# Kernel tuning notes

Hardware: AMD Instinct MI355X
Metric: run time of the kernel (lower is better)

The kernel has to match this reference:

```python
import jax, jax.numpy as jnp
import numpy as np

B, C, H, W, K = 32, 256, 32, 32, 1024
BETA = 0.25

def setup_inputs() -> dict:
    key = jax.random.key(0)
    k1, k2 = jax.random.split(key)
    z = jax.random.normal(k1, (B, C, H, W), dtype=jnp.float32)
    # torch init: uniform(-1/K, 1/K)
    embedding = jax.random.uniform(k2, (K, C), dtype=jnp.float32,
                                   minval=-1.0 / K, maxval=1.0 / K)
    return {"z": z, "embedding": embedding}

def reference(z, embedding):
    b, c, h, w = z.shape
    k = embedding.shape[0]
    # permute to [b,h,w,c] (contiguous)
    z_p = jnp.transpose(z, (0, 2, 3, 1))
    # Faithful to the torch code: the [b,h,w,c] contiguous buffer is .view()'d
    # as [b,1,c,h,w]; numpy/jnp reshape of the transposed array matches that.
    zz = z_p.reshape(b, c, h * w)                     # [b,c,hw] (reinterpreted)
    e = jax.lax.stop_gradient(embedding)              # torch uses .data here
    # ||e - z||^2 via dot-product trick, avoids [b,k,c,h,w] intermediate
    dist = (jnp.sum(e * e, axis=1)[None, :, None]
            + jnp.sum(zz * zz, axis=1)[:, None, :]
            - 2.0 * jnp.einsum('kc,bcn->bkn', e, zz))  # [b,k,hw]
    idx = jnp.argmin(dist, axis=1).reshape(b, h, w)    # [b,h,w]
    z_q = embedding[idx]                               # [b,h,w,c]
    loss = (jnp.mean((jax.lax.stop_gradient(z_q) - z_p) ** 2)
            + BETA * jnp.mean((z_q - jax.lax.stop_gradient(z_p)) ** 2))
    # straight-through estimator
    z_q_st = z_p + jax.lax.stop_gradient(z_q - z_p)
    return jnp.transpose(z_q_st, (0, 3, 1, 2)), idx, loss
```

## Files before the change

### kernel.cpp

```cpp
#include <hip/hip_runtime.h>
#include <stdint.h>

#define ZSIZE   8388608
#define NPIX    32768
#define IDX_OFF ZSIZE
#define LOSS_OFF (ZSIZE + NPIX)
#define ET_OFF  1024
#define E1_OFF  263168
#define ZT_OFF  394240
#define CAP     24
#define WWIN    6.0e-3f

using v8s = __attribute__((ext_vector_type(8))) short;
using v4f = __attribute__((ext_vector_type(4))) float;

__device__ __forceinline__ unsigned short bf16rne(float f) {
  unsigned u = __float_as_uint(f);
  return (unsigned short)((u + 0x7FFFu + ((u >> 16) & 1u)) >> 16);
}

__global__ __launch_bounds__(256) void ktr(const float* __restrict__ E,
                                           float* __restrict__ out) {
  __shared__ float tile[64][65];
  const int k0 = blockIdx.x * 64;
  const int c0 = blockIdx.y * 64;
  const int t = threadIdx.x;
  #pragma unroll
  for (int i = 0; i < 4; i++) {
    int f = t + 256 * i;
    int r = f >> 4, q = f & 15;
    float4 e = *(const float4*)(E + (k0 + r) * 256 + c0 + 4 * q);
    tile[r][4 * q + 0] = e.x; tile[r][4 * q + 1] = e.y;
    tile[r][4 * q + 2] = e.z; tile[r][4 * q + 3] = e.w;
  }
  __syncthreads();
  #pragma unroll
  for (int i = 0; i < 4; i++) {
    int f = t + 256 * i;
    int cr = f >> 4, kq = f & 15;
    float4 o;
    o.x = tile[4 * kq + 0][cr];
    o.y = tile[4 * kq + 1][cr];
    o.z = tile[4 * kq + 2][cr];
    o.w = tile[4 * kq + 3][cr];
    *(float4*)(out + ET_OFF + (c0 + cr) * 1024 + k0 + 4 * kq) = o;
  }
}

__global__ __launch_bounds__(256) void kse(float* __restrict__ out) {
  const int k = blockIdx.x * 256 + threadIdx.x;
  const float* Et = out + ET_OFF;
  float acc = 0.0f;
  #pragma unroll 8
  for (int c = 0; c < 256; c++) {
    float v = Et[c * 1024 + k];
    acc = __fadd_rn(acc, __fmul_rn(v, v));
  }
  out[k] = acc;
}

__global__ __launch_bounds__(256) void kes(const float* __restrict__ E,
                                           float* __restrict__ out) {
  unsigned short* e1s = (unsigned short*)(out + E1_OFF);
  const int tile = blockIdx.x;
  const int t = threadIdx.x;
  #pragma unroll
  for (int i = 0; i < 2; i++) {
    int chunk = t + 256 * i;
    int s = chunk >> 6, lane = chunk & 63;
    int r = lane & 15, h = (lane >> 4) & 3;
    const float* src = E + (16 * tile + r) * 256 + 8 * h + 32 * s;
    unsigned short o[8];
    #pragma unroll
    for (int j = 0; j < 8; j++) o[j] = bf16rne(src[j]);
    *(uint4*)(e1s + (size_t)tile * 4096 + (size_t)chunk * 8) = *(const uint4*)o;
  }
}

__global__ __launch_bounds__(256) void kzt(const float* __restrict__ z,
                                           float* __restrict__ out) {
  __shared__ float tile[16][1028];
  unsigned short* zt = (unsigned short*)(out + ZT_OFF);
  const int mg = blockIdx.x;
  const int b  = blockIdx.y;
  const int t = threadIdx.x;
  #pragma unroll
  for (int i = 0; i < 16; i++) {
    float4 v = *(const float4*)(z + (size_t)b * 262144 + (size_t)(mg * 16 + i) * 1024 + 4 * t);
    *(float4*)&tile[i][4 * t] = v;
  }
  __syncthreads();
  const int m = t & 15, w0 = (t >> 4) & 3;
  const int n = w0 * 256 + mg * 16 + m;
  #pragma unroll
  for (int i = 0; i < 8; i++) {
    int g = 4 * i + (t >> 6);
    int c0 = 8 * g;
    unsigned short o[8];
    #pragma unroll
    for (int j = 0; j < 8; j++)
      o[j] = bf16rne(tile[m][4 * (c0 + j) + w0]);
    *(uint4*)(zt + ((size_t)(b * 1024 + n)) * 256 + c0) = *(const uint4*)o;
  }
}

__global__ __launch_bounds__(256, 2) void kmain(const float* __restrict__ z,
                                                const float* __restrict__ E,
                                                float* __restrict__ out) {
  __shared__ __attribute__((aligned(16))) float szs[64];
  __shared__ __attribute__((aligned(16))) float dmins[64];
  __shared__ int   candK[64 * CAP];
  __shared__ float candD[64 * CAP];
  __shared__ int   cnt[64];

  const int t = threadIdx.x;
  const int ccg = blockIdx.x, b = blockIdx.y;
  const int cc0 = ccg * 16;
  const int lane = t & 63, w = t >> 6;
  const int r = t & 15, h = (t >> 4) & 3;
  const int w16r = w * 16 + r;
  const float* zb = z + (size_t)b * 262144;
  const float* se_g = out;
  const unsigned short* e1s = (const unsigned short*)(out + E1_OFF);
  const unsigned short* zt = (const unsigned short*)(out + ZT_OFF);

  if (t < 64) { cnt[t] = 0; dmins[t] = 3.4e38f; }

  if (lane < 16) {
    const int p = w * 16 + lane;
    const float* zp = zb + (cc0 + (p >> 2)) * 1024 + (p & 3);
    float a = 0.0f;
    #pragma unroll 8
    for (int c = 0; c < 256; c++) {
      float v = zp[4 * c];
      a = __fadd_rn(a, __fmul_rn(v, v));
    }
    szs[p] = a;
  }
  __syncthreads();

  float se16r[16];
  #pragma unroll
  for (int ti = 0; ti < 16; ti++) se16r[ti] = se_g[ti * 64 + w16r];

  #pragma unroll 1
  for (int Tp = 0; Tp < 2; Tp++) {
    const int T0 = 2 * Tp, T1 = T0 + 1;
    v8s A0[8], A1[8];
    {
      const unsigned short* a0p =
          zt + ((size_t)(b * 1024 + T0 * 256 + cc0 + r)) * 256 + 8 * h;
      const unsigned short* a1p = a0p + 256 * 256;
      #pragma unroll
      for (int s = 0; s < 8; s++) {
        A0[s] = *(const v8s*)(a0p + 32 * s);
        A1[s] = *(const v8s*)(a1p + 32 * s);
      }
    }
    float sz0[4], sz1[4], b0[4], b1[4];
    #pragma unroll
    for (int reg = 0; reg < 4; reg++) {
      sz0[reg] = szs[16 * h + 4 * reg + T0];
      sz1[reg] = szs[16 * h + 4 * reg + T1];
      b0[reg] = 3.4e38f; b1[reg] = 3.4e38f;
    }

    #pragma unroll 4
    for (int ti = 0; ti < 16; ti++) {
      const unsigned short* bb = e1s + (size_t)(4 * ti + w) * 4096 + (size_t)lane * 8;
      v4f acc0 = (v4f){0.f, 0.f, 0.f, 0.f};
      v4f acc1 = (v4f){0.f, 0.f, 0.f, 0.f};
      #pragma unroll
      for (int s = 0; s < 8; s++) {
        v8s B_ = *(const v8s*)(bb + 512 * s);
        acc0 = __builtin_amdgcn_mfma_f32_16x16x32_bf16(A0[s], B_, acc0, 0, 0, 0);
        acc1 = __builtin_amdgcn_mfma_f32_16x16x32_bf16(A1[s], B_, acc1, 0, 0, 0);
      }
      float se_l = se16r[ti];
      #pragma unroll
      for (int reg = 0; reg < 4; reg++) {
        b0[reg] = fminf(b0[reg], (se_l + sz0[reg]) - 2.0f * acc0[reg]);
        b1[reg] = fminf(b1[reg], (se_l + sz1[reg]) - 2.0f * acc1[reg]);
      }
    }
    #pragma unroll
    for (int reg = 0; reg < 4; reg++) {
      atomicMin((int*)&dmins[16 * h + 4 * reg + T0], __float_as_int(b0[reg]));
      atomicMin((int*)&dmins[16 * h + 4 * reg + T1], __float_as_int(b1[reg]));
    }
  }
  __syncthreads();

  #pragma unroll 1
  for (int Tp = 0; Tp < 2; Tp++) {
    const int T0 = 2 * Tp, T1 = T0 + 1;
    v8s A0[8], A1[8];
    {
      const unsigned short* a0p =
          zt + ((size_t)(b * 1024 + T0 * 256 + cc0 + r)) * 256 + 8 * h;
      const unsigned short* a1p = a0p + 256 * 256;
      #pragma unroll
      for (int s = 0; s < 8; s++) {
        A0[s] = *(const v8s*)(a0p + 32 * s);
        A1[s] = *(const v8s*)(a1p + 32 * s);
      }
    }
    float sz0[4], sz1[4], th0[4], th1[4];
    #pragma unroll
    for (int reg = 0; reg < 4; reg++) {
      sz0[reg] = szs[16 * h + 4 * reg + T0];
      sz1[reg] = szs[16 * h + 4 * reg + T1];
      th0[reg] = dmins[16 * h + 4 * reg + T0] + WWIN;
      th1[reg] = dmins[16 * h + 4 * reg + T1] + WWIN;
    }

    #pragma unroll 4
    for (int ti = 0; ti < 16; ti++) {
      const unsigned short* bb = e1s + (size_t)(4 * ti + w) * 4096 + (size_t)lane * 8;
      v4f acc0 = (v4f){0.f, 0.f, 0.f, 0.f};
      v4f acc1 = (v4f){0.f, 0.f, 0.f, 0.f};
      #pragma unroll
      for (int s = 0; s < 8; s++) {
        v8s B_ = *(const v8s*)(bb + 512 * s);
        acc0 = __builtin_amdgcn_mfma_f32_16x16x32_bf16(A0[s], B_, acc0, 0, 0, 0);
        acc1 = __builtin_amdgcn_mfma_f32_16x16x32_bf16(A1[s], B_, acc1, 0, 0, 0);
      }
      float se_l = se16r[ti];
      const int kl = ti * 64 + w16r;
      #pragma unroll
      for (int reg = 0; reg < 4; reg++) {
        float dd0 = (se_l + sz0[reg]) - 2.0f * acc0[reg];
        if (dd0 <= th0[reg]) {
          int p = 16 * h + 4 * reg + T0;
          int o = atomicAdd(&cnt[p], 1);
          if (o < CAP) { candK[p * CAP + o] = kl; candD[p * CAP + o] = dd0; }
        }
        float dd1 = (se_l + sz1[reg]) - 2.0f * acc1[reg];
        if (dd1 <= th1[reg]) {
          int p = 16 * h + 4 * reg + T1;
          int o = atomicAdd(&cnt[p], 1);
          if (o < CAP) { candK[p * CAP + o] = kl; candD[p * CAP + o] = dd1; }
        }
      }
    }
  }
  __syncthreads();

  for (int i = t; i < 64 * CAP; i += 256) {
    int p = i / CAP, slot = i - p * CAP;
    int cn = cnt[p];
    if (cn > CAP || slot >= cn) continue;
    int k = candK[i];
    const float* er = E + (size_t)k * 256;
    const float* zp = zb + (cc0 + (p >> 2)) * 1024 + (p & 3);
    float dot = 0.0f;
    #pragma unroll 8
    for (int c = 0; c < 256; c++)
      dot = __fmaf_rn(zp[4 * c], er[c], dot);
    candD[i] = __fsub_rn(__fadd_rn(se_g[k], szs[p]), __fmul_rn(2.0f, dot));
  }
  __syncthreads();

  if (t < 64) {
    int p = t, cn = cnt[p];
    if (cn <= CAP) {
      float bd = 3.4e38f; int bi = 0x7FFFFFFF;
      for (int s2 = 0; s2 < cn; s2++) {
        float d2 = candD[p * CAP + s2]; int k2 = candK[p * CAP + s2];
        if (d2 < bd || (d2 == bd && k2 < bi)) { bd = d2; bi = k2; }
      }
      int rr = p >> 2, w0 = p & 3;
      out[IDX_OFF + b * 1024 + (w0 * 256 + cc0 + rr)] = (float)bi;
    }
  }

  for (int p = 0; p < 64; p++) {
    if (cnt[p] > CAP && (p & 3) == w) {
      const float* zp = zb + (cc0 + (p >> 2)) * 1024 + (p & 3);
      float bd = 3.4e38f; int bi = 0x7FFFFFFF;
      for (int k = lane; k < 1024; k += 64) {
        const float* er = E + (size_t)k * 256;
        float dot = 0.0f;
        #pragma unroll 8
        for (int c = 0; c < 256; c++)
          dot = __fmaf_rn(zp[4 * c], er[c], dot);
        float d2 = __fsub_rn(__fadd_rn(se_g[k], szs[p]), __fmul_rn(2.0f, dot));
        if (d2 < bd || (d2 == bd && k < bi)) { bd = d2; bi = k; }
      }
      #pragma unroll
      for (int mm = 32; mm >= 1; mm >>= 1) {
        float d2 = __shfl_xor(bd, mm, 64);
        int i2 = __shfl_xor(bi, mm, 64);
        if (d2 < bd || (d2 == bd && i2 < bi)) { bd = d2; bi = i2; }
      }
      if (lane == 0) {
        int rr = p >> 2, w0 = p & 3;
        out[IDX_OFF + b * 1024 + (w0 * 256 + cc0 + rr)] = (float)bi;
      }
    }
  }
}

__global__ __launch_bounds__(256) void kout(const float* __restrict__ z,
                                            const float* __restrict__ E,
                                            float* __restrict__ out,
                                            float* __restrict__ ws) {
  __shared__ float red[4];
  const int t = threadIdx.x;
  const size_t g4 = (size_t)blockIdx.x * 256 + t;
  const size_t g = g4 * 4;
  const int b = (int)(g >> 18);
  const int c = (int)((g >> 10) & 255);
  const int n = (int)(g & 1023);

  float4 zp = *(const float4*)(z + g);
  float4 idxf = *(const float4*)(out + IDX_OFF + b * 1024 + n);
  int i0 = (int)idxf.x, i1 = (int)idxf.y, i2 = (int)idxf.z, i3 = (int)idxf.w;
  float q0 = E[i0 * 256 + c];
  float q1 = E[i1 * 256 + c];
  float q2 = E[i2 * 256 + c];
  float q3 = E[i3 * 256 + c];
  float d0 = __fsub_rn(q0, zp.x);
  float d1 = __fsub_rn(q1, zp.y);
  float d2 = __fsub_rn(q2, zp.z);
  float d3 = __fsub_rn(q3, zp.w);
  float4 o;
  o.x = __fadd_rn(zp.x, d0);
  o.y = __fadd_rn(zp.y, d1);
  o.z = __fadd_rn(zp.z, d2);
  o.w = __fadd_rn(zp.w, d3);
  *(float4*)(out + g) = o;

  float s = d0 * d0 + d1 * d1 + d2 * d2 + d3 * d3;
  #pragma unroll
  for (int off = 32; off > 0; off >>= 1) s += __shfl_down(s, off);
  if ((t & 63) == 0) red[t >> 6] = s;
  __syncthreads();
  if (t == 0) ws[blockIdx.x] = red[0] + red[1] + red[2] + red[3];
}

__global__ __launch_bounds__(256) void kfin(const float* __restrict__ ws,
                                            float* __restrict__ out) {
  __shared__ float red[4];
  const int t = threadIdx.x;
  float s = 0.0f;
  #pragma unroll
  for (int i = 0; i < 32; i++) s += ws[t + 256 * i];
  #pragma unroll
  for (int off = 32; off > 0; off >>= 1) s += __shfl_down(s, off);
  if ((t & 63) == 0) red[t >> 6] = s;
  __syncthreads();
  if (t == 0) {
    float S = red[0] + red[1] + red[2] + red[3];
    float m = S / 8388608.0f;
    out[LOSS_OFF] = __fadd_rn(m, __fmul_rn(0.25f, m));
  }
}

extern "C" void kernel_launch(void* const* d_in, const int* in_sizes, int n_in,
                              void* d_out, int out_size, void* d_ws, size_t ws_size,
                              hipStream_t stream) {
  const float* z = (const float*)d_in[0];
  const float* E = (const float*)d_in[1];
  float* out = (float*)d_out;
  float* ws = (float*)d_ws;

  ktr<<<dim3(16, 4), 256, 0, stream>>>(E, out);
  kse<<<dim3(4), 256, 0, stream>>>(out);
  kes<<<dim3(64), 256, 0, stream>>>(E, out);
  kzt<<<dim3(16, 32), 256, 0, stream>>>(z, out);
  kmain<<<dim3(16, 32), 256, 0, stream>>>(z, E, out);
  kout<<<dim3(8192), 256, 0, stream>>>(z, E, out, ws);
  kfin<<<dim3(1), 256, 0, stream>>>(ws, out);
}
```

Baseline: 304.4 us.

## Double kmain block to 512 threads and precompute pixel norms in kzt

```diff
diff --git a/kernel.cpp b/kernel.cpp
--- a/kernel.cpp
+++ b/kernel.cpp
@@ -8,6 +8,7 @@
 #define ET_OFF  1024
 #define E1_OFF  263168
 #define ZT_OFF  394240
+#define SZ_OFF  4588544
 #define CAP     24
 #define WWIN    6.0e-3f
 
@@ -81,6 +82,7 @@
                                            float* __restrict__ out) {
   __shared__ float tile[16][1028];
   unsigned short* zt = (unsigned short*)(out + ZT_OFF);
+  float* szg = out + SZ_OFF;
   const int mg = blockIdx.x;
   const int b  = blockIdx.y;
   const int t = threadIdx.x;
@@ -102,9 +104,19 @@
       o[j] = bf16rne(tile[m][4 * (c0 + j) + w0]);
     *(uint4*)(zt + ((size_t)(b * 1024 + n)) * 256 + c0) = *(const uint4*)o;
   }
-}
-
-__global__ __launch_bounds__(256, 2) void kmain(const float* __restrict__ z,
+  if (t < 64) {
+    const int ms = t >> 2, ws = t & 3;
+    float a = 0.0f;
+    #pragma unroll 8
+    for (int c = 0; c < 256; c++) {
+      float v = tile[ms][4 * c + ws];
+      a = __fadd_rn(a, __fmul_rn(v, v));
+    }
+    szg[b * 1024 + ws * 256 + mg * 16 + ms] = a;
+  }
+}
+
+__global__ __launch_bounds__(512, 2) void kmain(const float* __restrict__ z,
                                                 const float* __restrict__ E,
                                                 float* __restrict__ out) {
   __shared__ __attribute__((aligned(16))) float szs[64];
@@ -116,26 +128,20 @@
   const int t = threadIdx.x;
   const int ccg = blockIdx.x, b = blockIdx.y;
   const int cc0 = ccg * 16;
-  const int lane = t & 63, w = t >> 6;
+  const int lane = t & 63;
+  const int w = (t >> 6) & 3;
+  const int Tp = t >> 8;
   const int r = t & 15, h = (t >> 4) & 3;
   const int w16r = w * 16 + r;
   const float* zb = z + (size_t)b * 262144;
   const float* se_g = out;
   const unsigned short* e1s = (const unsigned short*)(out + E1_OFF);
   const unsigned short* zt = (const unsigned short*)(out + ZT_OFF);
-
-  if (t < 64) { cnt[t] = 0; dmins[t] = 3.4e38f; }
-
-  if (lane < 16) {
-    const int p = w * 16 + lane;
-    const float* zp = zb + (cc0 + (p >> 2)) * 1024 + (p & 3);
-    float a = 0.0f;
-    #pragma unroll 8
-    for (int c = 0; c < 256; c++) {
-      float v = zp[4 * c];
-      a = __fadd_rn(a, __fmul_rn(v, v));
-    }
-    szs[p] = a;
+  const float* szg = out + SZ_OFF;
+
+  if (t < 64) {
+    cnt[t] = 0; dmins[t] = 3.4e38f;
+    szs[t] = szg[b * 1024 + (t & 3) * 256 + cc0 + (t >> 2)];
   }
   __syncthreads();
 
@@ -143,27 +149,30 @@
   #pragma unroll
   for (int ti = 0; ti < 16; ti++) se16r[ti] = se_g[ti * 64 + w16r];
 
-  #pragma unroll 1
-  for (int Tp = 0; Tp < 2; Tp++) {
-    const int T0 = 2 * Tp, T1 = T0 + 1;
-    v8s A0[8], A1[8];
-    {
-      const unsigned short* a0p =
-          zt + ((size_t)(b * 1024 + T0 * 256 + cc0 + r)) * 256 + 8 * h;
-      const unsigned short* a1p = a0p + 256 * 256;
-      #pragma unroll
-      for (int s = 0; s < 8; s++) {
-        A0[s] = *(const v8s*)(a0p + 32 * s);
-        A1[s] = *(const v8s*)(a1p + 32 * s);
-      }
-    }
-    float sz0[4], sz1[4], b0[4], b1[4];
-    #pragma unroll
-    for (int reg = 0; reg < 4; reg++) {
-      sz0[reg] = szs[16 * h + 4 * reg + T0];
-      sz1[reg] = szs[16 * h + 4 * reg + T1];
-      b0[reg] = 3.4e38f; b1[reg] = 3.4e38f;
-    }
+  const int T0 = 2 * Tp, T1 = T0 + 1;
+
+  v8s A0[8], A1[8];
+  {
+    const unsigned short* a0p =
+        zt + ((size_t)(b * 1024 + T0 * 256 + cc0 + r)) * 256 + 8 * h;
+    const unsigned short* a1p = a0p + 256 * 256;
+    #pragma unroll
+    for (int s = 0; s < 8; s++) {
+      A0[s] = *(const v8s*)(a0p + 32 * s);
+      A1[s] = *(const v8s*)(a1p + 32 * s);
+    }
+  }
+  float sz0[4], sz1[4];
+  #pragma unroll
+  for (int reg = 0; reg < 4; reg++) {
+    sz0[reg] = szs[16 * h + 4 * reg + T0];
+    sz1[reg] = szs[16 * h + 4 * reg + T1];
+  }
+
+  {
+    float b0[4], b1[4];
+    #pragma unroll
+    for (int reg = 0; reg < 4; reg++) { b0[reg] = 3.4e38f; b1[reg] = 3.4e38f; }
 
     #pragma unroll 4
     for (int ti = 0; ti < 16; ti++) {
@@ -191,25 +200,10 @@
   }
   __syncthreads();
 
-  #pragma unroll 1
-  for (int Tp = 0; Tp < 2; Tp++) {
-    const int T0 = 2 * Tp, T1 = T0 + 1;
-    v8s A0[8], A1[8];
-    {
-      const unsigned short* a0p =
-          zt + ((size_t)(b * 1024 + T0 * 256 + cc0 + r)) * 256 + 8 * h;
-      const unsigned short* a1p = a0p + 256 * 256;
-      #pragma unroll
-      for (int s = 0; s < 8; s++) {
-        A0[s] = *(const v8s*)(a0p + 32 * s);
-        A1[s] = *(const v8s*)(a1p + 32 * s);
-      }
-    }
-    float sz0[4], sz1[4], th0[4], th1[4];
+  {
+    float th0[4], th1[4];
     #pragma unroll
     for (int reg = 0; reg < 4; reg++) {
-      sz0[reg] = szs[16 * h + 4 * reg + T0];
-      sz1[reg] = szs[16 * h + 4 * reg + T1];
       th0[reg] = dmins[16 * h + 4 * reg + T0] + WWIN;
       th1[reg] = dmins[16 * h + 4 * reg + T1] + WWIN;
     }
@@ -246,7 +240,7 @@
   }
   __syncthreads();
 
-  for (int i = t; i < 64 * CAP; i += 256) {
+  for (int i = t; i < 64 * CAP; i += 512) {
     int p = i / CAP, slot = i - p * CAP;
     int cn = cnt[p];
     if (cn > CAP || slot >= cn) continue;
@@ -275,7 +269,7 @@
   }
 
   for (int p = 0; p < 64; p++) {
-    if (cnt[p] > CAP && (p & 3) == w) {
+    if (cnt[p] > CAP && (p & 3) == w && Tp == 0) {
       const float* zp = zb + (cc0 + (p >> 2)) * 1024 + (p & 3);
       float bd = 3.4e38f; int bi = 0x7FFFFFFF;
       for (int k = lane; k < 1024; k += 64) {
@@ -369,7 +363,7 @@
   kse<<<dim3(4), 256, 0, stream>>>(out);
   kes<<<dim3(64), 256, 0, stream>>>(E, out);
   kzt<<<dim3(16, 32), 256, 0, stream>>>(z, out);
-  kmain<<<dim3(16, 32), 256, 0, stream>>>(z, E, out);
+  kmain<<<dim3(16, 32), 512, 0, stream>>>(z, E, out);
   kout<<<dim3(8192), 256, 0, stream>>>(z, E, out, ws);
   kfin<<<dim3(1), 256, 0, stream>>>(ws, out);
 }
```

Result: no change. 305.5 us (+0.3%).

## Double-buffer codebook tiles into LDS via async global_load_lds and precompute z norms

Applied to the files above, without the earlier changes.

```diff
diff --git a/kernel.cpp b/kernel.cpp
--- a/kernel.cpp
+++ b/kernel.cpp
@@ -8,6 +8,7 @@
 #define ET_OFF  1024
 #define E1_OFF  263168
 #define ZT_OFF  394240
+#define SZ_OFF  4588544
 #define CAP     24
 #define WWIN    6.0e-3f
 
@@ -17,6 +18,12 @@
 __device__ __forceinline__ unsigned short bf16rne(float f) {
   unsigned u = __float_as_uint(f);
   return (unsigned short)((u + 0x7FFFu + ((u >> 16) & 1u)) >> 16);
+}
+
+typedef const __attribute__((address_space(1))) void gv_t;
+typedef __attribute__((address_space(3))) void sv_t;
+__device__ __forceinline__ void gl_lds16(const void* g, void* l) {
+  __builtin_amdgcn_global_load_lds((gv_t*)g, (sv_t*)l, 16, 0, 0);
 }
 
 __global__ __launch_bounds__(256) void ktr(const float* __restrict__ E,
@@ -81,6 +88,7 @@
                                            float* __restrict__ out) {
   __shared__ float tile[16][1028];
   unsigned short* zt = (unsigned short*)(out + ZT_OFF);
+  float* szg = out + SZ_OFF;
   const int mg = blockIdx.x;
   const int b  = blockIdx.y;
   const int t = threadIdx.x;
@@ -102,14 +110,26 @@
       o[j] = bf16rne(tile[m][4 * (c0 + j) + w0]);
     *(uint4*)(zt + ((size_t)(b * 1024 + n)) * 256 + c0) = *(const uint4*)o;
   }
-}
-
-__global__ __launch_bounds__(256, 2) void kmain(const float* __restrict__ z,
+  if (t < 64) {
+    const int ms = t >> 2, ws = t & 3;
+    float a = 0.0f;
+    #pragma unroll 8
+    for (int c = 0; c < 256; c++) {
+      float v = tile[ms][4 * c + ws];
+      a = __fadd_rn(a, __fmul_rn(v, v));
+    }
+    szg[b * 1024 + ws * 256 + mg * 16 + ms] = a;
+  }
+}
+
+__global__ __launch_bounds__(256, 1) void kmain(const float* __restrict__ z,
                                                 const float* __restrict__ E,
                                                 float* __restrict__ out) {
+  __shared__ __attribute__((aligned(16))) short bufB[4][2][4096];
+  __shared__ __attribute__((aligned(16))) float ses[1024];
   __shared__ __attribute__((aligned(16))) float szs[64];
   __shared__ __attribute__((aligned(16))) float dmins[64];
-  __shared__ int   candK[64 * CAP];
+  __shared__ unsigned short candK[64 * CAP];
   __shared__ float candD[64 * CAP];
   __shared__ int   cnt[64];
 
@@ -123,25 +143,38 @@
   const float* se_g = out;
   const unsigned short* e1s = (const unsigned short*)(out + E1_OFF);
   const unsigned short* zt = (const unsigned short*)(out + ZT_OFF);
-
-  if (t < 64) { cnt[t] = 0; dmins[t] = 3.4e38f; }
-
-  if (lane < 16) {
-    const int p = w * 16 + lane;
-    const float* zp = zb + (cc0 + (p >> 2)) * 1024 + (p & 3);
-    float a = 0.0f;
-    #pragma unroll 8
-    for (int c = 0; c < 256; c++) {
-      float v = zp[4 * c];
-      a = __fadd_rn(a, __fmul_rn(v, v));
-    }
-    szs[p] = a;
-  }
-  __syncthreads();
-
-  float se16r[16];
-  #pragma unroll
-  for (int ti = 0; ti < 16; ti++) se16r[ti] = se_g[ti * 64 + w16r];
+  const float* szg = out + SZ_OFF;
+
+  if (t < 64) {
+    cnt[t] = 0; dmins[t] = 3.4e38f;
+    szs[t] = szg[b * 1024 + (t & 3) * 256 + cc0 + (t >> 2)];
+  }
+  *(float4*)&ses[4 * t] = *(const float4*)(se_g + 4 * t);
+  __syncthreads();
+
+#define STAGE(TAU, CUR)                                                       \
+  {                                                                           \
+    const unsigned short* sp_ = e1s + (size_t)(TAU) * 4096 + lane * 8;        \
+    short* dp_ = &bufB[w][CUR][lane * 8];                                     \
+    _Pragma("unroll")                                                         \
+    for (int s_ = 0; s_ < 8; s_++)                                            \
+      gl_lds16((const void*)(sp_ + 512 * s_), (void*)(dp_ + 512 * s_));       \
+  }
+
+#define MBODY(TI, CUR)                                                        \
+  {                                                                           \
+    const short* bb_ = &bufB[w][CUR][lane * 8];                               \
+    v4f acc0 = (v4f){0.f, 0.f, 0.f, 0.f};                                     \
+    v4f acc1 = (v4f){0.f, 0.f, 0.f, 0.f};                                     \
+    _Pragma("unroll")                                                         \
+    for (int s_ = 0; s_ < 8; s_++) {                                          \
+      v8s B_ = *(const v8s*)(bb_ + 512 * s_);                                 \
+      acc0 = __builtin_amdgcn_mfma_f32_16x16x32_bf16(A0[s_], B_, acc0, 0, 0, 0); \
+      acc1 = __builtin_amdgcn_mfma_f32_16x16x32_bf16(A1[s_], B_, acc1, 0, 0, 0); \
+    }                                                                         \
+    se_l = ses[(TI) * 64 + w16r];                                             \
+    ACC0 = acc0; ACC1 = acc1;                                                 \
+  }
 
   #pragma unroll 1
   for (int Tp = 0; Tp < 2; Tp++) {
@@ -165,23 +198,29 @@
       b0[reg] = 3.4e38f; b1[reg] = 3.4e38f;
     }
 
-    #pragma unroll 4
-    for (int ti = 0; ti < 16; ti++) {
-      const unsigned short* bb = e1s + (size_t)(4 * ti + w) * 4096 + (size_t)lane * 8;
-      v4f acc0 = (v4f){0.f, 0.f, 0.f, 0.f};
-      v4f acc1 = (v4f){0.f, 0.f, 0.f, 0.f};
-      #pragma unroll
-      for (int s = 0; s < 8; s++) {
-        v8s B_ = *(const v8s*)(bb + 512 * s);
-        acc0 = __builtin_amdgcn_mfma_f32_16x16x32_bf16(A0[s], B_, acc0, 0, 0, 0);
-        acc1 = __builtin_amdgcn_mfma_f32_16x16x32_bf16(A1[s], B_, acc1, 0, 0, 0);
-      }
-      float se_l = se16r[ti];
+    int cur = 0;
+    STAGE(w, 0);
+    v4f ACC0, ACC1; float se_l;
+    #pragma unroll 1
+    for (int ti = 0; ti < 15; ti++) {
+      STAGE(4 * (ti + 1) + w, cur ^ 1);
+      asm volatile("s_waitcnt vmcnt(8)" ::: "memory");
+      __builtin_amdgcn_sched_barrier(0);
+      MBODY(ti, cur);
       #pragma unroll
       for (int reg = 0; reg < 4; reg++) {
-        b0[reg] = fminf(b0[reg], (se_l + sz0[reg]) - 2.0f * acc0[reg]);
-        b1[reg] = fminf(b1[reg], (se_l + sz1[reg]) - 2.0f * acc1[reg]);
-      }
+        b0[reg] = fminf(b0[reg], (se_l + sz0[reg]) - 2.0f * ACC0[reg]);
+        b1[reg] = fminf(b1[reg], (se_l + sz1[reg]) - 2.0f * ACC1[reg]);
+      }
+      cur ^= 1;
+    }
+    asm volatile("s_waitcnt vmcnt(0)" ::: "memory");
+    __builtin_amdgcn_sched_barrier(0);
+    MBODY(15, cur);
+    #pragma unroll
+    for (int reg = 0; reg < 4; reg++) {
+      b0[reg] = fminf(b0[reg], (se_l + sz0[reg]) - 2.0f * ACC0[reg]);
+      b1[reg] = fminf(b1[reg], (se_l + sz1[reg]) - 2.0f * ACC1[reg]);
     }
     #pragma unroll
     for (int reg = 0; reg < 4; reg++) {
@@ -214,36 +253,40 @@
       th1[reg] = dmins[16 * h + 4 * reg + T1] + WWIN;
     }
 
-    #pragma unroll 4
+    int cur = 0;
+    STAGE(w, 0);
+    v4f ACC0, ACC1; float se_l;
+    #pragma unroll 1
     for (int ti = 0; ti < 16; ti++) {
-      const unsigned short* bb = e1s + (size_t)(4 * ti + w) * 4096 + (size_t)lane * 8;
-      v4f acc0 = (v4f){0.f, 0.f, 0.f, 0.f};
-      v4f acc1 = (v4f){0.f, 0.f, 0.f, 0.f};
-      #pragma unroll
-      for (int s = 0; s < 8; s++) {
-        v8s B_ = *(const v8s*)(bb + 512 * s);
-        acc0 = __builtin_amdgcn_mfma_f32_16x16x32_bf16(A0[s], B_, acc0, 0, 0, 0);
-        acc1 = __builtin_amdgcn_mfma_f32_16x16x32_bf16(A1[s], B_, acc1, 0, 0, 0);
-      }
-      float se_l = se16r[ti];
+      if (ti < 15) {
+        STAGE(4 * (ti + 1) + w, cur ^ 1);
+        asm volatile("s_waitcnt vmcnt(8)" ::: "memory");
+      } else {
+        asm volatile("s_waitcnt vmcnt(0)" ::: "memory");
+      }
+      __builtin_amdgcn_sched_barrier(0);
+      MBODY(ti, cur);
       const int kl = ti * 64 + w16r;
       #pragma unroll
       for (int reg = 0; reg < 4; reg++) {
-        float dd0 = (se_l + sz0[reg]) - 2.0f * acc0[reg];
+        float dd0 = (se_l + sz0[reg]) - 2.0f * ACC0[reg];
         if (dd0 <= th0[reg]) {
           int p = 16 * h + 4 * reg + T0;
           int o = atomicAdd(&cnt[p], 1);
-          if (o < CAP) { candK[p * CAP + o] = kl; candD[p * CAP + o] = dd0; }
+          if (o < CAP) { candK[p * CAP + o] = (unsigned short)kl; candD[p * CAP + o] = dd0; }
         }
-        float dd1 = (se_l + sz1[reg]) - 2.0f * acc1[reg];
+        float dd1 = (se_l + sz1[reg]) - 2.0f * ACC1[reg];
         if (dd1 <= th1[reg]) {
           int p = 16 * h + 4 * reg + T1;
           int o = atomicAdd(&cnt[p], 1);
-          if (o < CAP) { candK[p * CAP + o] = kl; candD[p * CAP + o] = dd1; }
+          if (o < CAP) { candK[p * CAP + o] = (unsigned short)kl; candD[p * CAP + o] = dd1; }
         }
       }
-    }
-  }
+      cur ^= 1;
+    }
+  }
+#undef MBODY
+#undef STAGE
   __syncthreads();
 
   for (int i = t; i < 64 * CAP; i += 256) {
```

New measurement: 283.4 us. -6.9%, faster.
